# Optimization experiments

Measured on AMD Instinct MI355X. Metric: run time of the kernel, lower is better.

The kernel has to match this reference:

```python
import jax, jax.numpy as jnp
import numpy as np

IN_CH = 63      # positionally-encoded points
IN_VIEWS = 63   # positionally-encoded view dirs (must equal IN_CH per source bug)
UNITS = 256
N = 131072
SKIPS = (4,)


def _linear_init(key, fan_in, fan_out):
    # torch nn.Linear default: U(-1/sqrt(fan_in), 1/sqrt(fan_in)) for W and b
    kw, kb = jax.random.split(key)
    bound = 1.0 / np.sqrt(fan_in)
    W = jax.random.uniform(kw, (fan_in, fan_out), jnp.float32, -bound, bound)
    b = jax.random.uniform(kb, (fan_out,), jnp.float32, -bound, bound)
    return W, b


def setup_inputs() -> dict:
    key = jax.random.key(0)
    keys = jax.random.split(key, 16)
    inp = {}
    inp["x"] = jax.random.normal(keys[0], (N, IN_CH + IN_VIEWS), jnp.float32)
    # 8 backbone layers; layer idx 5 consumes skip-concat of width UNITS+IN_CH
    fan_ins = [IN_CH] + [UNITS + IN_CH if (i - 1) in SKIPS else UNITS for i in range(1, 8)]
    for i, fi in enumerate(fan_ins):
        W, b = _linear_init(keys[1 + i], fi, UNITS)
        inp[f"W{i}"], inp[f"b{i}"] = W, b
    inp["Wf"], inp["bf"] = _linear_init(keys[9], UNITS, UNITS)          # linear_feature
    inp["Wa"], inp["ba"] = _linear_init(keys[10], UNITS, 1)             # linear_alpha
    inp["Wv"], inp["bv"] = _linear_init(keys[11], IN_CH + UNITS, UNITS // 2)  # linear_views[0]
    inp["Wr"], inp["br"] = _linear_init(keys[12], UNITS // 2, 3)        # linear_rgb
    return inp


def reference(x, W0, b0, W1, b1, W2, b2, W3, b3, W4, b4, W5, b5, W6, b6, W7, b7,
              Wf, bf, Wa, ba, Wv, bv, Wr, br):
    pts = x[..., :IN_CH]
    views = x[..., IN_CH:]
    Ws = (W0, W1, W2, W3, W4, W5, W6, W7)
    bs = (b0, b1, b2, b3, b4, b5, b6, b7)
    h = pts
    for idx in range(8):
        h = jax.nn.relu(h @ Ws[idx] + bs[idx])
        if idx in SKIPS:
            h = jnp.concatenate([pts, h], axis=-1)  # [N, IN_CH + UNITS]
    alpha = h @ Wa + ba                       # [N, 1]
    feature = h @ Wf + bf                     # [N, UNITS]
    hv = jnp.concatenate([feature, views], axis=-1)   # [N, UNITS + IN_VIEWS]
    hv = jax.nn.relu(hv @ Wv + bv)            # [N, UNITS//2]
    rgb = hv @ Wr + br                        # [N, 3]
    return jnp.concatenate([rgb, alpha], axis=-1)     # [N, 4]
```

## Files before the change

kernel.cpp:

```cpp
#include <hip/hip_runtime.h>
#include <hip/hip_bf16.h>


typedef __bf16 bfrag __attribute__((ext_vector_type(8)));
typedef float  f4    __attribute__((ext_vector_type(4)));
typedef unsigned short us4 __attribute__((ext_vector_type(4)));

constexpr int OFF_W0 = 0;
constexpr int OFF_W1 = 16384;
constexpr int OFF_W2 = 81920;
constexpr int OFF_W3 = 147456;
constexpr int OFF_W4 = 212992;
constexpr int OFF_W5 = 278528;
constexpr int OFF_W6 = 360448;
constexpr int OFF_W7 = 425984;
constexpr int OFF_WF = 491520;
constexpr int OFF_WV = 557056;
constexpr int OFF_WA = 598016;
constexpr int OFF_WR = 602112;
constexpr int WS_TOTAL = 604160;

__device__ __forceinline__ unsigned swz256(int row, int k) {
  return (unsigned)((row * 256 + k) ^ ((row & 7) << 3));
}
__device__ __forceinline__ unsigned swz64(int row, int k) {
  return (unsigned)((row * 64 + k) ^ ((row & 7) << 3));
}

template<int NCT, int NKS, int NCTS, int SSTR>
__device__ __forceinline__ void phase(f4 (&acc)[4][NCT],
    const unsigned short* __restrict__ src,
    const unsigned short* __restrict__ wt, int ks0, int ctb, int r0,
    int lane, int l15, int lk8) {
#pragma unroll
  for (int ks = 0; ks < NKS; ++ks) {
    const int kl = ks * 32 + lk8;
    bfrag a[4];
#pragma unroll
    for (int rt = 0; rt < 4; ++rt) {
      const int row = r0 + rt * 16 + l15;
      const unsigned idx = (SSTR == 256) ? swz256(row, kl) : swz64(row, kl);
      a[rt] = *(const bfrag*)(src + idx);
    }
    const unsigned short* wk =
        wt + ((size_t)(ks0 + ks) * NCTS + ctb) * 512 + lane * 8;
    constexpr int CH = (NCT < 4) ? NCT : 4;
#pragma unroll
    for (int c2 = 0; c2 < NCT; c2 += CH) {
      bfrag b[CH];
#pragma unroll
      for (int u = 0; u < CH; ++u)
        b[u] = *(const bfrag*)(wk + (size_t)(c2 + u) * 512);
#pragma unroll
      for (int u = 0; u < CH; ++u)
#pragma unroll
        for (int rt = 0; rt < 4; ++rt)
          acc[rt][c2 + u] = __builtin_amdgcn_mfma_f32_16x16x32_bf16(b[u], a[rt], acc[rt][c2 + u], 0, 0, 0);
    }
  }
}

template<int NCT>
__device__ __forceinline__ void init_acc(f4 (&acc)[4][NCT],
    const float* __restrict__ bias, int cb, int lk4) {
#pragma unroll
  for (int ct = 0; ct < NCT; ++ct) {
    const float4 bv = *(const float4*)(bias + cb + ct * 16 + lk4);
    f4 v = {bv.x, bv.y, bv.z, bv.w};
#pragma unroll
    for (int rt = 0; rt < 4; ++rt) acc[rt][ct] = v;
  }
}

template<bool RELU, int NCT>
__device__ __forceinline__ void store_h(f4 (&acc)[4][NCT],
    unsigned short* __restrict__ h, int cb, int r0, int l15, int lk4) {
#pragma unroll
  for (int ct = 0; ct < NCT; ++ct) {
    const int col0 = cb + ct * 16 + lk4;
#pragma unroll
    for (int rt = 0; rt < 4; ++rt) {
      us4 packed;
#pragma unroll
      for (int j = 0; j < 4; ++j) {
        float v = acc[rt][ct][j];
        if (RELU) v = fmaxf(v, 0.f);
        __bf16 bb = (__bf16)v;
        packed[j] = __builtin_bit_cast(unsigned short, bb);
      }
      *(us4*)(h + swz256(r0 + rt * 16 + l15, col0)) = packed;
    }
  }
}

__device__ __forceinline__ void stage_pts(const float* __restrict__ x,
    unsigned short* pv, int rowg0, int tid) {
  const int row = tid >> 2, seg = tid & 3;
  const float* xr = x + (size_t)(rowg0 + row) * 126;
  bfrag v0, v1;
#pragma unroll
  for (int q = 0; q < 4; ++q) {
    const int c = seg * 16 + 2 * q;
    float2 t = *(const float2*)(xr + c);
    v0[2 * q]     = (c     < 63) ? (__bf16)t.x : (__bf16)0.f;
    v0[2 * q + 1] = (c + 1 < 63) ? (__bf16)t.y : (__bf16)0.f;
  }
#pragma unroll
  for (int q = 0; q < 4; ++q) {
    const int c = seg * 16 + 8 + 2 * q;
    float2 t = *(const float2*)(xr + c);
    v1[2 * q]     = (c     < 63) ? (__bf16)t.x : (__bf16)0.f;
    v1[2 * q + 1] = (c + 1 < 63) ? (__bf16)t.y : (__bf16)0.f;
  }
  *(bfrag*)(pv + swz64(row, seg * 16))     = v0;
  *(bfrag*)(pv + swz64(row, seg * 16 + 8)) = v1;
}

__device__ __forceinline__ void stage_views(const float* __restrict__ x,
    unsigned short* pv, int rowg0, int tid) {
  const int row = tid >> 2, seg = tid & 3;
  const float* xr = x + (size_t)(rowg0 + row) * 126 + 63;
  bfrag w0, w1;
#pragma unroll
  for (int j = 0; j < 8; ++j) {
    const int c = seg * 16 + j;
    w0[j] = (c < 63) ? (__bf16)xr[c] : (__bf16)0.f;
  }
#pragma unroll
  for (int j = 0; j < 8; ++j) {
    const int c = seg * 16 + 8 + j;
    w1[j] = (c < 63) ? (__bf16)xr[c] : (__bf16)0.f;
  }
  *(bfrag*)(pv + swz64(row, seg * 16))     = w0;
  *(bfrag*)(pv + swz64(row, seg * 16 + 8)) = w1;
}

struct RepackArgs {
  const float *W0, *W1, *W2, *W3, *W4, *W5, *W6, *W7, *Wf, *Wv, *Wa, *Wr;
  unsigned short* ws;
};

__global__ void repack_kernel(RepackArgs a) {
  const int i = blockIdx.x * 256 + threadIdx.x;
  if (i >= WS_TOTAL) return;

  const float* src; int off, ncts, fanin, fanout; bool shift = false;
  int mode = 0;
  if      (i < OFF_W1) { src = a.W0; off = OFF_W0; ncts = 16; fanin = 63;  fanout = 256; }
  else if (i < OFF_W2) { src = a.W1; off = OFF_W1; ncts = 16; fanin = 256; fanout = 256; }
  else if (i < OFF_W3) { src = a.W2; off = OFF_W2; ncts = 16; fanin = 256; fanout = 256; }
  else if (i < OFF_W4) { src = a.W3; off = OFF_W3; ncts = 16; fanin = 256; fanout = 256; }
  else if (i < OFF_W5) { src = a.W4; off = OFF_W4; ncts = 16; fanin = 256; fanout = 256; }
  else if (i < OFF_W6) { src = a.W5; off = OFF_W5; ncts = 16; fanin = 319; fanout = 256; shift = true; }
  else if (i < OFF_W7) { src = a.W6; off = OFF_W6; ncts = 16; fanin = 256; fanout = 256; }
  else if (i < OFF_WF) { src = a.W7; off = OFF_W7; ncts = 16; fanin = 256; fanout = 256; }
  else if (i < OFF_WV) { src = a.Wf; off = OFF_WF; ncts = 16; fanin = 256; fanout = 256; }
  else if (i < OFF_WA) { src = a.Wv; off = OFF_WV; ncts = 8;  fanin = 319; fanout = 128; }
  else if (i < OFF_WR) { src = a.Wa; off = OFF_WA; ncts = 1;  fanin = 256; fanout = 1; mode = 1; }
  else                 { src = a.Wr; off = OFF_WR; ncts = 1;  fanin = 128; fanout = 3; mode = 2; }

  const int idx  = i - off;
  const int j    = idx & 7;
  const int lane = (idx >> 3) & 63;
  const int rem  = idx >> 9;
  const int ctg  = rem % ncts;
  const int ks   = rem / ncts;
  const int k    = ks * 32 + ((lane >> 4) << 3) + j;
  const int col  = ctg * 16 + (lane & 15);

  float v;
  if (mode == 1) {
    v = (col == 0 && k < fanin) ? src[k] : 0.f;
  } else if (mode == 2) {
    v = (col < 3 && k < fanin) ? src[(size_t)k * 3 + col] : 0.f;
  } else if (shift) {
    v = (k < 63) ? src[(size_t)k * 256 + col]
                 : ((k == 63) ? 0.f : src[(size_t)(k - 1) * 256 + col]);
  } else {
    v = (k < fanin) ? src[(size_t)k * fanout + col] : 0.f;
  }
  __bf16 bb = (__bf16)v;
  a.ws[i] = __builtin_bit_cast(unsigned short, bb);
}

struct MainArgs {
  const float* x;
  const unsigned short* ws;
  const float *b0, *b1, *b2, *b3, *b4, *b5, *b6, *b7;
  const float *bfc, *ba, *bv, *br;
  float* out;
};

__global__ __launch_bounds__(512, 2) void nerf_kernel(MainArgs A) {
  extern __shared__ unsigned short lds[];
  unsigned short* hA = lds;
  unsigned short* hB = lds + 128 * 256;
  unsigned short* pv = lds + 2 * 128 * 256;

  const int tid  = threadIdx.x;
  const int lane = tid & 63;
  const int wave = tid >> 6;
  const int wr   = wave >> 2;
  const int wc   = wave & 3;
  const int l15 = lane & 15;
  const int lk8 = (lane >> 4) << 3;
  const int lk4 = (lane >> 4) << 2;
  const int r0  = wr * 64;
  const int cb  = wc * 64;
  const int ctb = wc * 4;
  const int rowg0 = blockIdx.x * 128;
  const unsigned short* ws = A.ws;

  stage_pts(A.x, pv, rowg0, tid);
  __syncthreads();

  f4 acc[4][4];

  init_acc<4>(acc, A.b0, cb, lk4);
  phase<4, 2, 16, 64>(acc, pv, ws + OFF_W0, 0, ctb, r0, lane, l15, lk8);
  store_h<true, 4>(acc, hA, cb, r0, l15, lk4);
  __syncthreads();

  init_acc<4>(acc, A.b1, cb, lk4);
  phase<4, 8, 16, 256>(acc, hA, ws + OFF_W1, 0, ctb, r0, lane, l15, lk8);
  store_h<true, 4>(acc, hB, cb, r0, l15, lk4);
  __syncthreads();

  init_acc<4>(acc, A.b2, cb, lk4);
  phase<4, 8, 16, 256>(acc, hB, ws + OFF_W2, 0, ctb, r0, lane, l15, lk8);
  store_h<true, 4>(acc, hA, cb, r0, l15, lk4);
  __syncthreads();

  init_acc<4>(acc, A.b3, cb, lk4);
  phase<4, 8, 16, 256>(acc, hA, ws + OFF_W3, 0, ctb, r0, lane, l15, lk8);
  store_h<true, 4>(acc, hB, cb, r0, l15, lk4);
  __syncthreads();

  init_acc<4>(acc, A.b4, cb, lk4);
  phase<4, 8, 16, 256>(acc, hB, ws + OFF_W4, 0, ctb, r0, lane, l15, lk8);
  store_h<true, 4>(acc, hA, cb, r0, l15, lk4);
  __syncthreads();

  init_acc<4>(acc, A.b5, cb, lk4);
  phase<4, 2, 16, 64>(acc, pv, ws + OFF_W5, 0, ctb, r0, lane, l15, lk8);
  phase<4, 8, 16, 256>(acc, hA, ws + OFF_W5, 2, ctb, r0, lane, l15, lk8);
  store_h<true, 4>(acc, hB, cb, r0, l15, lk4);
  __syncthreads();

  stage_views(A.x, pv, rowg0, tid);

  init_acc<4>(acc, A.b6, cb, lk4);
  phase<4, 8, 16, 256>(acc, hB, ws + OFF_W6, 0, ctb, r0, lane, l15, lk8);
  store_h<true, 4>(acc, hA, cb, r0, l15, lk4);
  __syncthreads();

  init_acc<4>(acc, A.b7, cb, lk4);
  phase<4, 8, 16, 256>(acc, hA, ws + OFF_W7, 0, ctb, r0, lane, l15, lk8);
  store_h<true, 4>(acc, hB, cb, r0, l15, lk4);
  __syncthreads();

  if (wc == 0) {
    f4 accA[4][1];
#pragma unroll
    for (int rt = 0; rt < 4; ++rt) accA[rt][0] = (f4){0.f, 0.f, 0.f, 0.f};
    phase<1, 8, 1, 256>(accA, hB, ws + OFF_WA, 0, 0, r0, lane, l15, lk8);
    if (lk4 == 0) {
      const float ba0 = A.ba[0];
#pragma unroll
      for (int rt = 0; rt < 4; ++rt)
        A.out[(size_t)(rowg0 + r0 + rt * 16 + l15) * 4 + 3] = accA[rt][0][0] + ba0;
    }
  }

  init_acc<4>(acc, A.bfc, cb, lk4);
  phase<4, 8, 16, 256>(acc, hB, ws + OFF_WF, 0, ctb, r0, lane, l15, lk8);
  store_h<false, 4>(acc, hA, cb, r0, l15, lk4);
  __syncthreads();

  {
    f4 acc2[4][2];
    const int cb2 = wc * 32;
    init_acc<2>(acc2, A.bv, cb2, lk4);
    phase<2, 8, 8, 256>(acc2, hA, ws + OFF_WV, 0, wc * 2, r0, lane, l15, lk8);
    phase<2, 2, 8, 64>(acc2, pv, ws + OFF_WV, 8, wc * 2, r0, lane, l15, lk8);
    store_h<true, 2>(acc2, hB, cb2, r0, l15, lk4);
  }
  __syncthreads();

  if (wc == 0) {
    f4 accR[4][1];
#pragma unroll
    for (int rt = 0; rt < 4; ++rt) accR[rt][0] = (f4){0.f, 0.f, 0.f, 0.f};
    phase<1, 4, 1, 256>(accR, hB, ws + OFF_WR, 0, 0, r0, lane, l15, lk8);
    if (lk4 == 0) {
#pragma unroll
      for (int rt = 0; rt < 4; ++rt) {
        float* o = A.out + (size_t)(rowg0 + r0 + rt * 16 + l15) * 4;
#pragma unroll
        for (int j = 0; j < 3; ++j) o[j] = accR[rt][0][j] + A.br[j];
      }
    }
  }
}

extern "C" void kernel_launch(void* const* d_in, const int* in_sizes, int n_in,
                              void* d_out, int out_size, void* d_ws, size_t ws_size,
                              hipStream_t stream) {
  RepackArgs ra;
  ra.W0 = (const float*)d_in[1];  ra.W1 = (const float*)d_in[3];
  ra.W2 = (const float*)d_in[5];  ra.W3 = (const float*)d_in[7];
  ra.W4 = (const float*)d_in[9];  ra.W5 = (const float*)d_in[11];
  ra.W6 = (const float*)d_in[13]; ra.W7 = (const float*)d_in[15];
  ra.Wf = (const float*)d_in[17]; ra.Wv = (const float*)d_in[21];
  ra.Wa = (const float*)d_in[19]; ra.Wr = (const float*)d_in[23];
  ra.ws = (unsigned short*)d_ws;
  repack_kernel<<<(WS_TOTAL + 255) / 256, 256, 0, stream>>>(ra);

  MainArgs ma;
  ma.x   = (const float*)d_in[0];
  ma.ws  = (const unsigned short*)d_ws;
  ma.b0  = (const float*)d_in[2];  ma.b1 = (const float*)d_in[4];
  ma.b2  = (const float*)d_in[6];  ma.b3 = (const float*)d_in[8];
  ma.b4  = (const float*)d_in[10]; ma.b5 = (const float*)d_in[12];
  ma.b6  = (const float*)d_in[14]; ma.b7 = (const float*)d_in[16];
  ma.bfc = (const float*)d_in[18];
  ma.ba  = (const float*)d_in[20];
  ma.bv  = (const float*)d_in[22];
  ma.br  = (const float*)d_in[24];
  ma.out = (float*)d_out;

  const int n    = in_sizes[0] / 126;
  const int grid = n / 128;

  hipFuncSetAttribute(reinterpret_cast<const void*>(nerf_kernel),
                      hipFuncAttributeMaxDynamicSharedMemorySize, 147456);
  nerf_kernel<<<grid, 512, 147456, stream>>>(ma);
}
```

Baseline: 199.9 us.

## Switch to 32x32x16 MFMA with 4-wave blocks and single LDS activation buffer

Replaces the 16x16x32 bf16 MFMA tiling with 32x32x16 MFMA. The weights are repacked into the matching fragment layout, and the block shrinks to 4 waves, each covering all 128 rows and 64 output columns. The ping-pong activation buffers become one in-place buffer, guarded by an extra barrier between the reads and the writeback, which cuts LDS use from 144KB to 80KB per block. The goal is fewer MFMA issues, higher throughput per instruction and less LDS pressure, at the cost of an added barrier per layer and larger accumulators per wave. The alpha and rgb heads now also run as 32x32 tiles in which only one or three columns are meaningful.

```diff
diff --git a/kernel.cpp b/kernel.cpp
--- a/kernel.cpp
+++ b/kernel.cpp
@@ -3,7 +3,7 @@
 
 
 typedef __bf16 bfrag __attribute__((ext_vector_type(8)));
-typedef float  f4    __attribute__((ext_vector_type(4)));
+typedef float  f16v  __attribute__((ext_vector_type(16)));
 typedef unsigned short us4 __attribute__((ext_vector_type(4)));
 
 constexpr int OFF_W0 = 0;
@@ -17,122 +17,129 @@
 constexpr int OFF_WF = 491520;
 constexpr int OFF_WV = 557056;
 constexpr int OFF_WA = 598016;
-constexpr int OFF_WR = 602112;
-constexpr int WS_TOTAL = 604160;
-
-__device__ __forceinline__ unsigned swz256(int row, int k) {
-  return (unsigned)((row * 256 + k) ^ ((row & 7) << 3));
-}
-__device__ __forceinline__ unsigned swz64(int row, int k) {
+constexpr int OFF_WR = 606208;
+constexpr int WS_TOTAL = 610304;
+
+__device__ __forceinline__ unsigned swzH(int row, int k) {
+  return (unsigned)((row * 256 + k) ^ ((row & 31) << 3));
+}
+__device__ __forceinline__ unsigned swzP(int row, int k) {
   return (unsigned)((row * 64 + k) ^ ((row & 7) << 3));
 }
 
-template<int NCT, int NKS, int NCTS, int SSTR>
-__device__ __forceinline__ void phase(f4 (&acc)[4][NCT],
+template<int NCT, int NKS, int NCTS, bool PV>
+__device__ __forceinline__ void phase32(f16v (&acc)[4][NCT],
     const unsigned short* __restrict__ src,
-    const unsigned short* __restrict__ wt, int ks0, int ctb, int r0,
-    int lane, int l15, int lk8) {
+    const unsigned short* __restrict__ wt, int ks0, int ctb,
+    int lane, int l31, int hi8) {
 #pragma unroll
   for (int ks = 0; ks < NKS; ++ks) {
-    const int kl = ks * 32 + lk8;
+    const int kl = ks * 16 + hi8;
     bfrag a[4];
 #pragma unroll
     for (int rt = 0; rt < 4; ++rt) {
-      const int row = r0 + rt * 16 + l15;
-      const unsigned idx = (SSTR == 256) ? swz256(row, kl) : swz64(row, kl);
+      const int row = rt * 32 + l31;
+      const unsigned idx = PV ? swzP(row, kl) : swzH(row, kl);
       a[rt] = *(const bfrag*)(src + idx);
     }
     const unsigned short* wk =
         wt + ((size_t)(ks0 + ks) * NCTS + ctb) * 512 + lane * 8;
-    constexpr int CH = (NCT < 4) ? NCT : 4;
-#pragma unroll
-    for (int c2 = 0; c2 < NCT; c2 += CH) {
-      bfrag b[CH];
-#pragma unroll
-      for (int u = 0; u < CH; ++u)
-        b[u] = *(const bfrag*)(wk + (size_t)(c2 + u) * 512);
-#pragma unroll
-      for (int u = 0; u < CH; ++u)
-#pragma unroll
-        for (int rt = 0; rt < 4; ++rt)
-          acc[rt][c2 + u] = __builtin_amdgcn_mfma_f32_16x16x32_bf16(b[u], a[rt], acc[rt][c2 + u], 0, 0, 0);
-    }
+    bfrag b[NCT];
+#pragma unroll
+    for (int u = 0; u < NCT; ++u)
+      b[u] = *(const bfrag*)(wk + (size_t)u * 512);
+#pragma unroll
+    for (int u = 0; u < NCT; ++u)
+#pragma unroll
+      for (int rt = 0; rt < 4; ++rt)
+        acc[rt][u] = __builtin_amdgcn_mfma_f32_32x32x16_bf16(b[u], a[rt], acc[rt][u], 0, 0, 0);
   }
 }
 
 template<int NCT>
-__device__ __forceinline__ void init_acc(f4 (&acc)[4][NCT],
-    const float* __restrict__ bias, int cb, int lk4) {
+__device__ __forceinline__ void init_acc32(f16v (&acc)[4][NCT],
+    const float* __restrict__ bias, int cb, int hi4) {
 #pragma unroll
   for (int ct = 0; ct < NCT; ++ct) {
-    const float4 bv = *(const float4*)(bias + cb + ct * 16 + lk4);
-    f4 v = {bv.x, bv.y, bv.z, bv.w};
+    f16v v;
+#pragma unroll
+    for (int q = 0; q < 4; ++q) {
+      const float4 bv = *(const float4*)(bias + cb + ct * 32 + q * 8 + hi4);
+      v[q * 4 + 0] = bv.x; v[q * 4 + 1] = bv.y;
+      v[q * 4 + 2] = bv.z; v[q * 4 + 3] = bv.w;
+    }
 #pragma unroll
     for (int rt = 0; rt < 4; ++rt) acc[rt][ct] = v;
   }
 }
 
+template<int NCT>
+__device__ __forceinline__ void zero_acc32(f16v (&acc)[4][NCT]) {
+#pragma unroll
+  for (int rt = 0; rt < 4; ++rt)
+#pragma unroll
+    for (int ct = 0; ct < NCT; ++ct)
+#pragma unroll
+      for (int e = 0; e < 16; ++e) acc[rt][ct][e] = 0.f;
+}
+
 template<bool RELU, int NCT>
-__device__ __forceinline__ void store_h(f4 (&acc)[4][NCT],
-    unsigned short* __restrict__ h, int cb, int r0, int l15, int lk4) {
-#pragma unroll
-  for (int ct = 0; ct < NCT; ++ct) {
-    const int col0 = cb + ct * 16 + lk4;
+__device__ __forceinline__ void store_h32(f16v (&acc)[4][NCT],
+    unsigned short* __restrict__ h, int cb, int l31, int hi4) {
+#pragma unroll
+  for (int ct = 0; ct < NCT; ++ct)
 #pragma unroll
     for (int rt = 0; rt < 4; ++rt) {
-      us4 packed;
-#pragma unroll
-      for (int j = 0; j < 4; ++j) {
-        float v = acc[rt][ct][j];
-        if (RELU) v = fmaxf(v, 0.f);
-        __bf16 bb = (__bf16)v;
-        packed[j] = __builtin_bit_cast(unsigned short, bb);
+      const int row = rt * 32 + l31;
+#pragma unroll
+      for (int q = 0; q < 4; ++q) {
+        us4 p;
+#pragma unroll
+        for (int j = 0; j < 4; ++j) {
+          float v = acc[rt][ct][q * 4 + j];
+          if (RELU) v = fmaxf(v, 0.f);
+          __bf16 bb = (__bf16)v;
+          p[j] = __builtin_bit_cast(unsigned short, bb);
+        }
+        *(us4*)(h + swzH(row, cb + ct * 32 + q * 8 + hi4)) = p;
       }
-      *(us4*)(h + swz256(r0 + rt * 16 + l15, col0)) = packed;
-    }
-  }
+    }
 }
 
 __device__ __forceinline__ void stage_pts(const float* __restrict__ x,
     unsigned short* pv, int rowg0, int tid) {
-  const int row = tid >> 2, seg = tid & 3;
+  const int row = tid >> 1, seg = tid & 1;
   const float* xr = x + (size_t)(rowg0 + row) * 126;
-  bfrag v0, v1;
-#pragma unroll
-  for (int q = 0; q < 4; ++q) {
-    const int c = seg * 16 + 2 * q;
-    float2 t = *(const float2*)(xr + c);
-    v0[2 * q]     = (c     < 63) ? (__bf16)t.x : (__bf16)0.f;
-    v0[2 * q + 1] = (c + 1 < 63) ? (__bf16)t.y : (__bf16)0.f;
-  }
-#pragma unroll
-  for (int q = 0; q < 4; ++q) {
-    const int c = seg * 16 + 8 + 2 * q;
-    float2 t = *(const float2*)(xr + c);
-    v1[2 * q]     = (c     < 63) ? (__bf16)t.x : (__bf16)0.f;
-    v1[2 * q + 1] = (c + 1 < 63) ? (__bf16)t.y : (__bf16)0.f;
-  }
-  *(bfrag*)(pv + swz64(row, seg * 16))     = v0;
-  *(bfrag*)(pv + swz64(row, seg * 16 + 8)) = v1;
+#pragma unroll
+  for (int g = 0; g < 4; ++g) {
+    const int k0 = seg * 32 + g * 8;
+    bfrag v;
+#pragma unroll
+    for (int p = 0; p < 4; ++p) {
+      const int c = k0 + 2 * p;
+      float2 t = *(const float2*)(xr + c);
+      v[2 * p]     = (c     < 63) ? (__bf16)t.x : (__bf16)0.f;
+      v[2 * p + 1] = (c + 1 < 63) ? (__bf16)t.y : (__bf16)0.f;
+    }
+    *(bfrag*)(pv + swzP(row, k0)) = v;
+  }
 }
 
 __device__ __forceinline__ void stage_views(const float* __restrict__ x,
     unsigned short* pv, int rowg0, int tid) {
-  const int row = tid >> 2, seg = tid & 3;
+  const int row = tid >> 1, seg = tid & 1;
   const float* xr = x + (size_t)(rowg0 + row) * 126 + 63;
-  bfrag w0, w1;
-#pragma unroll
-  for (int j = 0; j < 8; ++j) {
-    const int c = seg * 16 + j;
-    w0[j] = (c < 63) ? (__bf16)xr[c] : (__bf16)0.f;
-  }
-#pragma unroll
-  for (int j = 0; j < 8; ++j) {
-    const int c = seg * 16 + 8 + j;
-    w1[j] = (c < 63) ? (__bf16)xr[c] : (__bf16)0.f;
-  }
-  *(bfrag*)(pv + swz64(row, seg * 16))     = w0;
-  *(bfrag*)(pv + swz64(row, seg * 16 + 8)) = w1;
+#pragma unroll
+  for (int g = 0; g < 4; ++g) {
+    const int k0 = seg * 32 + g * 8;
+    bfrag v;
+#pragma unroll
+    for (int j = 0; j < 8; ++j) {
+      const int c = k0 + j;
+      v[j] = (c < 63) ? (__bf16)xr[c] : (__bf16)0.f;
+    }
+    *(bfrag*)(pv + swzP(row, k0)) = v;
+  }
 }
 
 struct RepackArgs {
@@ -146,18 +153,18 @@
 
   const float* src; int off, ncts, fanin, fanout; bool shift = false;
   int mode = 0;
-  if      (i < OFF_W1) { src = a.W0; off = OFF_W0; ncts = 16; fanin = 63;  fanout = 256; }
-  else if (i < OFF_W2) { src = a.W1; off = OFF_W1; ncts = 16; fanin = 256; fanout = 256; }
-  else if (i < OFF_W3) { src = a.W2; off = OFF_W2; ncts = 16; fanin = 256; fanout = 256; }
-  else if (i < OFF_W4) { src = a.W3; off = OFF_W3; ncts = 16; fanin = 256; fanout = 256; }
-  else if (i < OFF_W5) { src = a.W4; off = OFF_W4; ncts = 16; fanin = 256; fanout = 256; }
-  else if (i < OFF_W6) { src = a.W5; off = OFF_W5; ncts = 16; fanin = 319; fanout = 256; shift = true; }
-  else if (i < OFF_W7) { src = a.W6; off = OFF_W6; ncts = 16; fanin = 256; fanout = 256; }
-  else if (i < OFF_WF) { src = a.W7; off = OFF_W7; ncts = 16; fanin = 256; fanout = 256; }
-  else if (i < OFF_WV) { src = a.Wf; off = OFF_WF; ncts = 16; fanin = 256; fanout = 256; }
-  else if (i < OFF_WA) { src = a.Wv; off = OFF_WV; ncts = 8;  fanin = 319; fanout = 128; }
-  else if (i < OFF_WR) { src = a.Wa; off = OFF_WA; ncts = 1;  fanin = 256; fanout = 1; mode = 1; }
-  else                 { src = a.Wr; off = OFF_WR; ncts = 1;  fanin = 128; fanout = 3; mode = 2; }
+  if      (i < OFF_W1) { src = a.W0; off = OFF_W0; ncts = 8; fanin = 63;  fanout = 256; }
+  else if (i < OFF_W2) { src = a.W1; off = OFF_W1; ncts = 8; fanin = 256; fanout = 256; }
+  else if (i < OFF_W3) { src = a.W2; off = OFF_W2; ncts = 8; fanin = 256; fanout = 256; }
+  else if (i < OFF_W4) { src = a.W3; off = OFF_W3; ncts = 8; fanin = 256; fanout = 256; }
+  else if (i < OFF_W5) { src = a.W4; off = OFF_W4; ncts = 8; fanin = 256; fanout = 256; }
+  else if (i < OFF_W6) { src = a.W5; off = OFF_W5; ncts = 8; fanin = 319; fanout = 256; shift = true; }
+  else if (i < OFF_W7) { src = a.W6; off = OFF_W6; ncts = 8; fanin = 256; fanout = 256; }
+  else if (i < OFF_WF) { src = a.W7; off = OFF_W7; ncts = 8; fanin = 256; fanout = 256; }
+  else if (i < OFF_WV) { src = a.Wf; off = OFF_WF; ncts = 8; fanin = 256; fanout = 256; }
+  else if (i < OFF_WA) { src = a.Wv; off = OFF_WV; ncts = 4; fanin = 319; fanout = 128; }
+  else if (i < OFF_WR) { src = a.Wa; off = OFF_WA; ncts = 1; fanin = 256; fanout = 1; mode = 1; }
+  else                 { src = a.Wr; off = OFF_WR; ncts = 1; fanin = 128; fanout = 3; mode = 2; }
 
   const int idx  = i - off;
   const int j    = idx & 7;
@@ -165,8 +172,8 @@
   const int rem  = idx >> 9;
   const int ctg  = rem % ncts;
   const int ks   = rem / ncts;
-  const int k    = ks * 32 + ((lane >> 4) << 3) + j;
-  const int col  = ctg * 16 + (lane & 15);
+  const int k    = ks * 16 + ((lane >> 5) << 3) + j;
+  const int col  = ctg * 32 + (lane & 31);
 
   float v;
   if (mode == 1) {
@@ -191,111 +198,112 @@
   float* out;
 };
 
-__global__ __launch_bounds__(512, 2) void nerf_kernel(MainArgs A) {
+__global__ __launch_bounds__(256, 2) void nerf_kernel(MainArgs A) {
   extern __shared__ unsigned short lds[];
-  unsigned short* hA = lds;
-  unsigned short* hB = lds + 128 * 256;
-  unsigned short* pv = lds + 2 * 128 * 256;
+  unsigned short* h  = lds;
+  unsigned short* pv = lds + 128 * 256;
 
   const int tid  = threadIdx.x;
   const int lane = tid & 63;
   const int wave = tid >> 6;
-  const int wr   = wave >> 2;
-  const int wc   = wave & 3;
-  const int l15 = lane & 15;
-  const int lk8 = (lane >> 4) << 3;
-  const int lk4 = (lane >> 4) << 2;
-  const int r0  = wr * 64;
-  const int cb  = wc * 64;
-  const int ctb = wc * 4;
+  const int l31  = lane & 31;
+  const int hi8  = (lane >> 5) << 3;
+  const int hi4  = (lane >> 5) << 2;
+  const int cb   = wave * 64;
+  const int ctb  = wave * 2;
   const int rowg0 = blockIdx.x * 128;
   const unsigned short* ws = A.ws;
 
   stage_pts(A.x, pv, rowg0, tid);
   __syncthreads();
 
-  f4 acc[4][4];
-
-  init_acc<4>(acc, A.b0, cb, lk4);
-  phase<4, 2, 16, 64>(acc, pv, ws + OFF_W0, 0, ctb, r0, lane, l15, lk8);
-  store_h<true, 4>(acc, hA, cb, r0, l15, lk4);
-  __syncthreads();
-
-  init_acc<4>(acc, A.b1, cb, lk4);
-  phase<4, 8, 16, 256>(acc, hA, ws + OFF_W1, 0, ctb, r0, lane, l15, lk8);
-  store_h<true, 4>(acc, hB, cb, r0, l15, lk4);
-  __syncthreads();
-
-  init_acc<4>(acc, A.b2, cb, lk4);
-  phase<4, 8, 16, 256>(acc, hB, ws + OFF_W2, 0, ctb, r0, lane, l15, lk8);
-  store_h<true, 4>(acc, hA, cb, r0, l15, lk4);
-  __syncthreads();
-
-  init_acc<4>(acc, A.b3, cb, lk4);
-  phase<4, 8, 16, 256>(acc, hA, ws + OFF_W3, 0, ctb, r0, lane, l15, lk8);
-  store_h<true, 4>(acc, hB, cb, r0, l15, lk4);
-  __syncthreads();
-
-  init_acc<4>(acc, A.b4, cb, lk4);
-  phase<4, 8, 16, 256>(acc, hB, ws + OFF_W4, 0, ctb, r0, lane, l15, lk8);
-  store_h<true, 4>(acc, hA, cb, r0, l15, lk4);
-  __syncthreads();
-
-  init_acc<4>(acc, A.b5, cb, lk4);
-  phase<4, 2, 16, 64>(acc, pv, ws + OFF_W5, 0, ctb, r0, lane, l15, lk8);
-  phase<4, 8, 16, 256>(acc, hA, ws + OFF_W5, 2, ctb, r0, lane, l15, lk8);
-  store_h<true, 4>(acc, hB, cb, r0, l15, lk4);
-  __syncthreads();
-
+  f16v acc[4][2];
+
+  init_acc32<2>(acc, A.b0, cb, hi4);
+  phase32<2, 4, 8, true>(acc, pv, ws + OFF_W0, 0, ctb, lane, l31, hi8);
+  store_h32<true, 2>(acc, h, cb, l31, hi4);
+  __syncthreads();
+
+  init_acc32<2>(acc, A.b1, cb, hi4);
+  phase32<2, 16, 8, false>(acc, h, ws + OFF_W1, 0, ctb, lane, l31, hi8);
+  __syncthreads();
+  store_h32<true, 2>(acc, h, cb, l31, hi4);
+  __syncthreads();
+
+  init_acc32<2>(acc, A.b2, cb, hi4);
+  phase32<2, 16, 8, false>(acc, h, ws + OFF_W2, 0, ctb, lane, l31, hi8);
+  __syncthreads();
+  store_h32<true, 2>(acc, h, cb, l31, hi4);
+  __syncthreads();
+
+  init_acc32<2>(acc, A.b3, cb, hi4);
+  phase32<2, 16, 8, false>(acc, h, ws + OFF_W3, 0, ctb, lane, l31, hi8);
+  __syncthreads();
+  store_h32<true, 2>(acc, h, cb, l31, hi4);
+  __syncthreads();
+
+  init_acc32<2>(acc, A.b4, cb, hi4);
+  phase32<2, 16, 8, false>(acc, h, ws + OFF_W4, 0, ctb, lane, l31, hi8);
+  __syncthreads();
+  store_h32<true, 2>(acc, h, cb, l31, hi4);
+  __syncthreads();
+
+  init_acc32<2>(acc, A.b5, cb, hi4);
+  phase32<2, 4, 8, true>(acc, pv, ws + OFF_W5, 0, ctb, lane, l31, hi8);
+  phase32<2, 16, 8, false>(acc, h, ws + OFF_W5, 4, ctb, lane, l31, hi8);
+  __syncthreads();
+  store_h32<true, 2>(acc, h, cb, l31, hi4);
   stage_views(A.x, pv, rowg0, tid);
-
-  init_acc<4>(acc, A.b6, cb, lk4);
-  phase<4, 8, 16, 256>(acc, hB, ws + OFF_W6, 0, ctb, r0, lane, l15, lk8);
-  store_h<true, 4>(acc, hA, cb, r0, l15, lk4);
-  __syncthreads();
-
-  init_acc<4>(acc, A.b7, cb, lk4);
-  phase<4, 8, 16, 256>(acc, hA, ws + OFF_W7, 0, ctb, r0, lane, l15, lk8);
-  store_h<true, 4>(acc, hB, cb, r0, l15, lk4);
-  __syncthreads();
-
-  if (wc == 0) {
-    f4 accA[4][1];
-#pragma unroll
-    for (int rt = 0; rt < 4; ++rt) accA[rt][0] = (f4){0.f, 0.f, 0.f, 0.f};
-    phase<1, 8, 1, 256>(accA, hB, ws + OFF_WA, 0, 0, r0, lane, l15, lk8);
-    if (lk4 == 0) {
+  __syncthreads();
+
+  init_acc32<2>(acc, A.b6, cb, hi4);
+  phase32<2, 16, 8, false>(acc, h, ws + OFF_W6, 0, ctb, lane, l31, hi8);
+  __syncthreads();
+  store_h32<true, 2>(acc, h, cb, l31, hi4);
+  __syncthreads();
+
+  init_acc32<2>(acc, A.b7, cb, hi4);
+  phase32<2, 16, 8, false>(acc, h, ws + OFF_W7, 0, ctb, lane, l31, hi8);
+  __syncthreads();
+  store_h32<true, 2>(acc, h, cb, l31, hi4);
+  __syncthreads();
+
+  if (wave == 0) {
+    f16v accA[4][1];
+    zero_acc32<1>(accA);
+    phase32<1, 16, 1, false>(accA, h, ws + OFF_WA, 0, 0, lane, l31, hi8);
+    if (hi8 == 0) {
       const float ba0 = A.ba[0];
 #pragma unroll
       for (int rt = 0; rt < 4; ++rt)
-        A.out[(size_t)(rowg0 + r0 + rt * 16 + l15) * 4 + 3] = accA[rt][0][0] + ba0;
-    }
-  }
-
-  init_acc<4>(acc, A.bfc, cb, lk4);
-  phase<4, 8, 16, 256>(acc, hB, ws + OFF_WF, 0, ctb, r0, lane, l15, lk8);
-  store_h<false, 4>(acc, hA, cb, r0, l15, lk4);
+        A.out[(size_t)(rowg0 + rt * 32 + l31) * 4 + 3] = accA[rt][0][0] + ba0;
+    }
+  }
+
+  init_acc32<2>(acc, A.bfc, cb, hi4);
+  phase32<2, 16, 8, false>(acc, h, ws + OFF_WF, 0, ctb, lane, l31, hi8);
+  __syncthreads();
+  store_h32<false, 2>(acc, h, cb, l31, hi4);
   __syncthreads();
 
   {
-    f4 acc2[4][2];
-    const int cb2 = wc * 32;
-    init_acc<2>(acc2, A.bv, cb2, lk4);
-    phase<2, 8, 8, 256>(acc2, hA, ws + OFF_WV, 0, wc * 2, r0, lane, l15, lk8);
-    phase<2, 2, 8, 64>(acc2, pv, ws + OFF_WV, 8, wc * 2, r0, lane, l15, lk8);
-    store_h<true, 2>(acc2, hB, cb2, r0, l15, lk4);
-  }
-  __syncthreads();
-
-  if (wc == 0) {
-    f4 accR[4][1];
-#pragma unroll
-    for (int rt = 0; rt < 4; ++rt) accR[rt][0] = (f4){0.f, 0.f, 0.f, 0.f};
-    phase<1, 4, 1, 256>(accR, hB, ws + OFF_WR, 0, 0, r0, lane, l15, lk8);
-    if (lk4 == 0) {
+    f16v accV[4][1];
+    init_acc32<1>(accV, A.bv, wave * 32, hi4);
+    phase32<1, 16, 4, false>(accV, h, ws + OFF_WV, 0, wave, lane, l31, hi8);
+    phase32<1, 4, 4, true>(accV, pv, ws + OFF_WV, 16, wave, lane, l31, hi8);
+    __syncthreads();
+    store_h32<true, 1>(accV, h, wave * 32, l31, hi4);
+  }
+  __syncthreads();
+
+  if (wave == 0) {
+    f16v accR[4][1];
+    zero_acc32<1>(accR);
+    phase32<1, 8, 1, false>(accR, h, ws + OFF_WR, 0, 0, lane, l31, hi8);
+    if (hi8 == 0) {
 #pragma unroll
       for (int rt = 0; rt < 4; ++rt) {
-        float* o = A.out + (size_t)(rowg0 + r0 + rt * 16 + l15) * 4;
+        float* o = A.out + (size_t)(rowg0 + rt * 32 + l31) * 4;
 #pragma unroll
         for (int j = 0; j < 3; ++j) o[j] = accR[rt][0][j] + A.br[j];
       }
@@ -333,6 +341,6 @@
   const int grid = n / 128;
 
   hipFuncSetAttribute(reinterpret_cast<const void*>(nerf_kernel),
-                      hipFuncAttributeMaxDynamicSharedMemorySize, 147456);
-  nerf_kernel<<<grid, 512, 147456, stream>>>(ma);
-}
+                      hipFuncAttributeMaxDynamicSharedMemorySize, 81920);
+  nerf_kernel<<<grid, 256, 81920, stream>>>(ma);
+}
```

New measurement: 229.5 us. 14.8% more time.
